# Optimization experiments

Measured on AMD Instinct MI355X. Metric: run time of the kernel, lower is better.

The kernel has to match this reference:

```python
import jax, jax.numpy as jnp
import numpy as np

F32 = jnp.float32

def denorm_px(pts, H, W):
    # kornia denormalize_pixel_coordinates: [-1,1] -> pixel
    x = (pts[..., 0] + 1.0) * (W - 1) * 0.5
    y = (pts[..., 1] + 1.0) * (H - 1) * 0.5
    return jnp.stack([x, y], axis=-1)

def norm_px(pts, H, W):
    x = pts[..., 0] * 2.0 / (W - 1) - 1.0
    y = pts[..., 1] * 2.0 / (H - 1) - 1.0
    return jnp.stack([x, y], axis=-1)

def conv2d_same(x, k, mode):
    # depthwise 2d conv, 'same' output, border via jnp.pad mode
    kh, kw = k.shape
    ph, pw = kh // 2, kw // 2
    xp = jnp.pad(x, ((0, 0), (0, 0), (ph, ph), (pw, pw)), mode=mode)
    C = x.shape[1]
    kern = jnp.broadcast_to(k[None, None], (C, 1, kh, kw)).astype(x.dtype)
    return jax.lax.conv_general_dilated(xp, kern, (1, 1), 'VALID',
        dimension_numbers=('NCHW', 'OIHW', 'NCHW'), feature_group_count=C)

def nms2d(x, k=5):
    p = k // 2
    m = jax.lax.reduce_window(x, -jnp.inf, jax.lax.max, (1, 1, k, k), (1, 1, 1, 1),
                              [(0, 0), (0, 0), (p, p), (p, p)])
    return jnp.where(x == m, x, 0.0)

def gaussian_kernel2d(ksize=7, sigma=1.0):
    ax = jnp.arange(ksize, dtype=F32) - (ksize - 1) / 2.0
    g = jnp.exp(-0.5 * (ax / sigma) ** 2)
    g = g / g.sum()
    return jnp.outer(g, g)

def gftt_response(gray):
    # kornia CornerGFTT: normalized sobel grads, blurred structure tensor, min-eig
    sx = jnp.array([[-1, 0, 1], [-2, 0, 2], [-1, 0, 1]], F32) / 8.0
    gx = conv2d_same(gray, sx, 'edge')
    gy = conv2d_same(gray, sx.T, 'edge')
    g = gaussian_kernel2d(7, 1.0)
    dx2 = conv2d_same(gx * gx, g, 'reflect')
    dy2 = conv2d_same(gy * gy, g, 'reflect')
    dxy = conv2d_same(gx * gy, g, 'reflect')
    tr = dx2 + dy2
    disc = jnp.sqrt(jnp.clip((dx2 - dy2) ** 2 + 4.0 * dxy ** 2, 0.0))
    return 0.5 * (tr - disc)

def laplacian5(x):
    k = jnp.ones((5, 5), F32).at[2, 2].set(1.0 - 25.0)
    k = k / jnp.abs(k).sum()  # kornia normalized laplacian kernel
    return conv2d_same(x, k, 'reflect')

def pairwise_project(pts, depths, poses, K):
    # pts [B,N,2] normalized; poses [B,4,4] cam-to-world
    # returns proj [B(dst),B(src),N,2] normalized + vis [B,B,N]
    B, N, _ = pts.shape
    H, W = depths.shape[-2:]
    px = denorm_px(pts, H, W)
    xi = jnp.clip(jnp.round(px[..., 0]), 0, W - 1).astype(jnp.int32)
    yi = jnp.clip(jnp.round(px[..., 1]), 0, H - 1).astype(jnp.int32)
    d = depths[jnp.arange(B)[:, None], 0, yi, xi]  # [B,N]
    Kinv = jnp.linalg.inv(K)
    hom = jnp.concatenate([px, jnp.ones_like(px[..., :1])], axis=-1)
    cam = (hom @ Kinv.T) * d[..., None]  # [B,N,3]
    R, t = poses[:, :3, :3], poses[:, :3, 3]
    world = jnp.einsum('bij,bnj->bni', R, cam) + t[:, None]
    diff = world[None] - t[:, None, None]  # [i,j,n,3]
    cam2 = jnp.einsum('iab,ijna->ijnb', R, diff)  # R_i^T (world - t_i)
    uvw = cam2 @ K.T
    z = uvw[..., 2]
    zs = jnp.where(jnp.abs(z) > 1e-6, z, 1e-6)
    u, v = uvw[..., 0] / zs, uvw[..., 1] / zs
    vis = (z > 0.1) & (u >= 0) & (u <= W - 1) & (v >= 0) & (v <= H - 1)
    return norm_px(jnp.stack([u, v], -1), H, W), vis

def pairwise_cosine_inter(x, y, eps=1e-8):
    xx = jnp.sum(x * x, -1)
    yy = jnp.sum(y * y, -1)
    xy = jnp.einsum('amd,bnd->abmn', x, y)
    den = jnp.sqrt(jnp.clip(xx[:, None, :, None] * yy[None, :, None, :], eps * eps))
    return xy / den

def pairwise_cosine_intra(x, y, eps=1e-8):
    xx = jnp.sum(x * x, -1)
    yy = jnp.sum(y * y, -1)
    xy = jnp.einsum('bmd,bnd->bmn', x, y)
    den = jnp.sqrt(jnp.clip(xx[..., :, None] * yy[..., None, :], eps * eps))
    return xy / den

def distinction_loss(desc):
    return jnp.maximum(pairwise_cosine_intra(desc, desc), 0.0).mean()

def match_loss(desc, points, proj, vis, H, W, radius=1.0):
    B, N, _ = points.shape
    src = denorm_px(jax.lax.stop_gradient(points), H, W)  # [b,m,2]
    dst = denorm_px(jax.lax.stop_gradient(proj), H, W)  # [a,b,n,2]
    x2 = jnp.sum(src * src, -1)  # [b,m]
    y2 = jnp.sum(dst * dst, -1)  # [a,b,n]
    xy = jnp.einsum('bmd,abnd->abmn', src, dst)
    dist = jnp.sqrt(jnp.clip(x2[None, :, :, None] + y2[:, :, None, :] - 2.0 * xy, 0.0))
    valid = vis[:, :, :, None]  # torch: dist[invis rows] = nan -> excluded from both masks
    tri = jnp.triu(jnp.ones((N, N), bool), 1)
    pcos = pairwise_cosine_inter(desc, desc)
    mpos = (dist <= radius) & tri & valid
    mneg = (dist > radius) & tri & valid
    pos_mean = jnp.sum(jnp.where(mpos, pcos, 0.0)) / jnp.maximum(mpos.sum(), 1)
    neg_mean = jnp.sum(jnp.where(mneg, pcos, 0.0)) / jnp.maximum(mneg.sum(), 1)
    return 1.0 - pos_mean + neg_mean

def get_corner_target(imgs, depths, poses, K, num_corners=500, radius=8):
    B, _, H, W = imgs.shape
    gray = 0.299 * imgs[:, 0:1] + 0.587 * imgs[:, 1:2] + 0.114 * imgs[:, 2:3]
    corners = nms2d(gftt_response(gray), 5)
    # MaxPool(8, return_indices) + MaxUnpool(8): keep only per-8x8-block max
    xr = corners.reshape(B, 1, H // radius, radius, W // radius, radius)
    bm = xr.max(axis=(3, 5), keepdims=True)
    keep = jnp.where(xr == bm, xr, 0.0).reshape(B, 1, H, W)
    values, idx = jax.lax.top_k(keep.reshape(B, -1), num_corners)  # [B,Nc]
    coords = jnp.stack([idx % W, idx // W], axis=2).astype(F32)  # (x,y)
    coords = norm_px(coords, H, W)
    proj, vis = pairwise_project(coords, depths, poses, K)  # [B,B,Nc,2]
    proj = jnp.where(vis[..., None], proj, -2.0)
    comb = jnp.transpose(proj, (1, 0, 2, 3)).reshape(B, B * num_corners, 2)
    px = jnp.round(denorm_px(comb, H, W)).astype(jnp.int32)
    wf = px[..., 0].reshape(-1)
    hf = px[..., 1].reshape(-1)
    bf = jnp.repeat(jnp.arange(B), B * num_corners)
    vals = jnp.tile(values.reshape(-1), B)
    mask = (wf >= 0) & (hf >= 0) & (wf < W) & (hf < H)
    vals = jnp.where(mask, vals, 0.0)
    wf = jnp.clip(wf, 0, W - 1)
    hf = jnp.clip(hf, 0, H - 1)
    target = jnp.zeros_like(corners).at[bf, 0, hf, wf].max(vals)
    target = nms2d(target, 5)
    return jax.lax.stop_gradient((target > 0).astype(F32))

def score_loss(scores, imgs, depths, poses, K):
    target = get_corner_target(imgs, depths, poses, K)
    p = jnp.clip(scores, 1e-12, 1.0 - 1e-12)
    bce = -(target * jnp.log(p) + (1.0 - target) * jnp.log(1.0 - p)).mean()
    lap = laplacian5(scores)
    return bce + (scores * jnp.exp(-lap)).mean() * 10.0

def featurenet_loss(descriptors, points, pointness, depths_dense, poses, K, imgs):
    beta = (1.0, 0.5, 1.0)
    H, W = pointness.shape[2], pointness.shape[3]
    distinction = distinction_loss(descriptors)
    cornerness = score_loss(pointness, imgs, depths_dense, poses, K)
    proj_pts, vis = pairwise_project(points, depths_dense, poses, K)
    match = match_loss(descriptors, points, proj_pts, vis, H, W, radius=1.0)
    return beta[0] * distinction + beta[1] * cornerness + beta[2] * match

def setup_inputs() -> dict:
    key = jax.random.key(0)
    ks = jax.random.split(key, 6)
    B, N, D, H, W = 6, 1024, 128, 320, 320
    descriptors = jax.random.normal(ks[0], (B, N, D), F32)
    points = jax.random.uniform(ks[1], (B, N, 2), F32, -0.9, 0.9)
    pointness = jax.random.uniform(ks[2], (B, 1, H, W), F32, 1e-3, 1.0 - 1e-3)
    depths_dense = jax.random.uniform(ks[3], (B, 1, H, W), F32, 1.0, 6.0)
    t = jax.random.uniform(ks[4], (B, 3), F32, -0.2, 0.2)
    poses = jnp.tile(jnp.eye(4, dtype=F32), (B, 1, 1)).at[:, :3, 3].set(t)
    K = jnp.array([[float(W), 0.0, W / 2.0], [0.0, float(W), H / 2.0], [0.0, 0.0, 1.0]], F32)
    imgs = jax.random.uniform(ks[5], (B, 3, H, W), F32)
    return dict(descriptors=descriptors, points=points, pointness=pointness,
                depths_dense=depths_dense, poses=poses, K=K, imgs=imgs)

def reference(descriptors, points, pointness, depths_dense, poses, K, imgs):
    return featurenet_loss(descriptors, points, pointness, depths_dense, poses, K, imgs)
```

## Files before the change

### kernel.cpp

```cpp
#include <hip/hip_runtime.h>
#include <stdint.h>

#define BB 6
#define NPTS 1024
#define DD 128
#define HH 320
#define WW 320
#define NC 500
#define HWsz (HH*WW)
#define CAP 2048
#define NBLK ((HH/8)*(WW/8))
#define TX 32
#define TY 8
#define NSLOT 64

typedef __attribute__((ext_vector_type(8))) short bf16x8;
typedef __attribute__((ext_vector_type(4))) float f32x4;

__device__ __forceinline__ int clampi(int v, int lo, int hi){ return v<lo?lo:(v>hi?hi:v); }
__device__ __forceinline__ int refl(int p, int L){ if(p<0)p=-p; if(p>=L)p=2*L-2-p; return p; }

__device__ __forceinline__ float wave_sum(float v){
  #pragma unroll
  for (int o = 32; o > 0; o >>= 1) v += __shfl_xor(v, o, 64);
  return v;
}
__device__ __forceinline__ double wave_sumd(double v){
  #pragma unroll
  for (int o = 32; o > 0; o >>= 1) v += __shfl_xor(v, o, 64);
  return v;
}
__device__ __forceinline__ float wave_max(float v){
  #pragma unroll
  for (int o = 32; o > 0; o >>= 1) v = fmaxf(v, __shfl_xor(v, o, 64));
  return v;
}

__device__ __constant__ float GW[7] = {
  0.0044330481f, 0.0540055850f, 0.2420362300f, 0.3990502700f,
  0.2420362300f, 0.0540055850f, 0.0044330481f };

struct Proj { float u, v; int vis; };

__device__ Proj project_point(float ptx, float pty, int jsrc, int itgt,
                              const float* __restrict__ depths,
                              const float* __restrict__ poses,
                              const float* __restrict__ Km)
{
  float pxx = ((ptx + 1.0f)*(float)(WW-1))*0.5f;
  float pxy = ((pty + 1.0f)*(float)(HH-1))*0.5f;
  float rx = rintf(pxx), ry = rintf(pxy);
  rx = fminf(fmaxf(rx, 0.f), (float)(WW-1));
  ry = fminf(fmaxf(ry, 0.f), (float)(HH-1));
  int xi = (int)rx, yi = (int)ry;
  float d = depths[(size_t)jsrc*HWsz + yi*WW + xi];
  float a00=Km[0],a01=Km[1],a02=Km[2],a10=Km[3],a11=Km[4],a12=Km[5],a20=Km[6],a21=Km[7],a22=Km[8];
  float det = a00*(a11*a22 - a12*a21) - a01*(a10*a22 - a12*a20) + a02*(a10*a21 - a11*a20);
  float id_ = 1.0f/det;
  float i00 = (a11*a22 - a12*a21)*id_;
  float i01 = (a02*a21 - a01*a22)*id_;
  float i02 = (a01*a12 - a02*a11)*id_;
  float i10 = (a12*a20 - a10*a22)*id_;
  float i11 = (a00*a22 - a02*a20)*id_;
  float i12 = (a02*a10 - a00*a12)*id_;
  float i20 = (a10*a21 - a11*a20)*id_;
  float i21 = (a01*a20 - a00*a21)*id_;
  float i22 = (a00*a11 - a01*a10)*id_;
  float c0 = (i00*pxx + i01*pxy + i02)*d;
  float c1 = (i10*pxx + i11*pxy + i12)*d;
  float c2 = (i20*pxx + i21*pxy + i22)*d;
  const float* Pj = poses + (size_t)jsrc*16;
  float w0 = Pj[0]*c0 + Pj[1]*c1 + Pj[2]*c2  + Pj[3];
  float w1 = Pj[4]*c0 + Pj[5]*c1 + Pj[6]*c2  + Pj[7];
  float w2 = Pj[8]*c0 + Pj[9]*c1 + Pj[10]*c2 + Pj[11];
  const float* Pi = poses + (size_t)itgt*16;
  float dx = w0 - Pi[3], dy = w1 - Pi[7], dz = w2 - Pi[11];
  float e0 = Pi[0]*dx + Pi[4]*dy + Pi[8]*dz;
  float e1 = Pi[1]*dx + Pi[5]*dy + Pi[9]*dz;
  float e2 = Pi[2]*dx + Pi[6]*dy + Pi[10]*dz;
  float uu = a00*e0 + a01*e1 + a02*e2;
  float vv = a10*e0 + a11*e1 + a12*e2;
  float zz = a20*e0 + a21*e1 + a22*e2;
  float zs = (fabsf(zz) > 1e-6f) ? zz : 1e-6f;
  Proj r;
  r.u = uu/zs; r.v = vv/zs;
  r.vis = (zz > 0.1f) && (r.u >= 0.f) && (r.u <= (float)(WW-1)) && (r.v >= 0.f) && (r.v <= (float)(HH-1));
  return r;
}

__global__ void k_gray(const float* __restrict__ imgs, float* __restrict__ gray){
  int t = blockIdx.x*blockDim.x + threadIdx.x;
  if (t >= BB*HWsz) return;
  int b = t / HWsz, p = t - b*HWsz;
  const float* base = imgs + (size_t)b*3*HWsz;
  gray[t] = 0.299f*base[p] + 0.587f*base[HWsz+p] + 0.114f*base[2*HWsz+p];
}

__global__ void k_sobel(const float* __restrict__ gray, float* __restrict__ gxx,
                        float* __restrict__ gyy, float* __restrict__ gxy){
  int t = blockIdx.x*blockDim.x + threadIdx.x;
  if (t >= BB*HWsz) return;
  int b = t / HWsz, p = t - b*HWsz;
  int y = p / WW, x = p - y*WW;
  const float* g = gray + (size_t)b*HWsz;
  int ym = clampi(y-1,0,HH-1), yp = clampi(y+1,0,HH-1);
  int xm = clampi(x-1,0,WW-1), xp = clampi(x+1,0,WW-1);
  float g00 = g[ym*WW+xm], g01 = g[ym*WW+x], g02 = g[ym*WW+xp];
  float g10 = g[y*WW+xm],                    g12 = g[y*WW+xp];
  float g20 = g[yp*WW+xm], g21 = g[yp*WW+x], g22 = g[yp*WW+xp];
  float gx = 0.125f*(g02-g00) + 0.25f*(g12-g10) + 0.125f*(g22-g20);
  float gy = 0.125f*(g20-g00) + 0.25f*(g21-g01) + 0.125f*(g22-g02);
  gxx[t] = gx*gx; gyy[t] = gy*gy; gxy[t] = gx*gy;
}

__global__ __launch_bounds__(256) void k_gauss_resp(const float* __restrict__ gxx,
        const float* __restrict__ gyy, const float* __restrict__ gxy, float* __restrict__ resp){
  __shared__ float lxx[TY+6][TX+6], lyy[TY+6][TX+6], lxy[TY+6][TX+6];
  int b = blockIdx.z;
  int x0 = blockIdx.x*TX, y0 = blockIdx.y*TY;
  const float* axx = gxx + (size_t)b*HWsz;
  const float* ayy = gyy + (size_t)b*HWsz;
  const float* axy = gxy + (size_t)b*HWsz;
  const int W2 = TX+6, H2 = TY+6;
  for (int i = threadIdx.x; i < H2*W2; i += 256){
    int ly = i / W2, lx = i - ly*W2;
    int gy = refl(y0 - 3 + ly, HH), gx = refl(x0 - 3 + lx, WW);
    size_t off = (size_t)gy*WW + gx;
    lxx[ly][lx] = axx[off]; lyy[ly][lx] = ayy[off]; lxy[ly][lx] = axy[off];
  }
  __syncthreads();
  int tx = threadIdx.x & (TX-1), ty = threadIdx.x / TX;
  float sxx=0.f, syy=0.f, sxy=0.f;
  #pragma unroll
  for (int i=0;i<7;++i){
    float wr = GW[i];
    #pragma unroll
    for (int j=0;j<7;++j){
      float wc = wr*GW[j];
      sxx += wc*lxx[ty+i][tx+j];
      syy += wc*lyy[ty+i][tx+j];
      sxy += wc*lxy[ty+i][tx+j];
    }
  }
  float tr = sxx+syy, df = sxx-syy;
  float disc = sqrtf(fmaxf(df*df + 4.f*sxy*sxy, 0.f));
  resp[(size_t)b*HWsz + (size_t)(y0+ty)*WW + (x0+tx)] = 0.5f*(tr - disc);
}

__global__ __launch_bounds__(256) void k_nms5(const float* __restrict__ resp, float* __restrict__ keep){
  __shared__ float lr[TY+4][TX+4];
  int b = blockIdx.z;
  int x0 = blockIdx.x*TX, y0 = blockIdx.y*TY;
  const float* rb = resp + (size_t)b*HWsz;
  const int W2 = TX+4, H2 = TY+4;
  for (int i = threadIdx.x; i < H2*W2; i += 256){
    int ly = i / W2, lx = i - ly*W2;
    int gy = y0 - 2 + ly, gx = x0 - 2 + lx;
    lr[ly][lx] = (gy >= 0 && gy < HH && gx >= 0 && gx < WW) ? rb[(size_t)gy*WW + gx] : -1e30f;
  }
  __syncthreads();
  int tx = threadIdx.x & (TX-1), ty = threadIdx.x / TX;
  float m = -1e30f;
  #pragma unroll
  for (int dy=0; dy<5; ++dy)
    #pragma unroll
    for (int dx=0; dx<5; ++dx) m = fmaxf(m, lr[ty+dy][tx+dx]);
  float r = lr[ty+2][tx+2];
  keep[(size_t)b*HWsz + (size_t)(y0+ty)*WW + (x0+tx)] = (r == m) ? r : 0.f;
}

__global__ void k_blockmax_compact(const float* __restrict__ keep,
        unsigned long long* __restrict__ ckeys, unsigned int* __restrict__ ccnt){
  int gw = (blockIdx.x*(int)blockDim.x + (int)threadIdx.x) >> 6;
  int lane = threadIdx.x & 63;
  if (gw >= BB*NBLK) return;
  int b = gw / NBLK; int r = gw - b*NBLK;
  int by = r / (WW/8), bx = r - by*(WW/8);
  int yy = by*8 + (lane >> 3), xx2 = bx*8 + (lane & 7);
  float v = keep[(size_t)b*HWsz + (size_t)yy*WW + xx2];
  float bm = wave_max(v);
  if (!(bm > 0.f)) return;
  unsigned long long mask = __ballot(v == bm);
  if (v == bm){
    unsigned long long key =
      ((unsigned long long)__float_as_uint(bm) << 32) |
      (unsigned long long)(0xFFFFFFFFu - (unsigned int)(yy*WW + xx2));
    int rank = __popcll(mask & ((1ull << lane) - 1ull));
    if (rank == 0){
      ckeys[(size_t)b*CAP + r] = key;
    } else {
      unsigned int slot = NBLK + atomicAdd(&ccnt[b], 1u);
      if (slot < CAP) ckeys[(size_t)b*CAP + slot] = key;
    }
  }
}

__global__ __launch_bounds__(1024) void k_top500(const unsigned long long* __restrict__ ckeys,
        float* __restrict__ cpts, float* __restrict__ cvals){
  __shared__ unsigned long long sk[CAP];
  int b = blockIdx.x;
  int tid = threadIdx.x;
  for (int i = tid; i < CAP; i += 1024)
    sk[i] = ckeys[(size_t)b*CAP + i];
  __syncthreads();
  for (int k = 2; k <= CAP; k <<= 1){
    for (int j = k >> 1; j > 0; j >>= 1){
      for (int i = tid; i < CAP; i += 1024){
        int l = i ^ j;
        if (l > i){
          unsigned long long A = sk[i], Bv = sk[l];
          bool up = ((i & k) == 0);
          if ((A > Bv) == up){ sk[i] = Bv; sk[l] = A; }
        }
      }
      __syncthreads();
    }
  }
  if (tid < NC){
    unsigned long long key = sk[CAP-1-tid];
    float val = __uint_as_float((unsigned int)(key >> 32));
    size_t o = (size_t)b*NC + tid;
    if (val > 0.f){
      unsigned int idx = 0xFFFFFFFFu - (unsigned int)(key & 0xFFFFFFFFull);
      float fx = (float)(idx % WW), fy = (float)(idx / WW);
      cpts[o*2+0] = (fx*2.0f)/(float)(WW-1) - 1.0f;
      cpts[o*2+1] = (fy*2.0f)/(float)(HH-1) - 1.0f;
      cvals[o] = val;
    } else {
      cpts[o*2+0] = __int_as_float(0x7fc00000);
      cpts[o*2+1] = __int_as_float(0x7fc00000);
      cvals[o] = 0.f;
    }
  }
}

__global__ void k_corner_scatter(const float* __restrict__ cpts, const float* __restrict__ cvals,
        const float* __restrict__ depths, const float* __restrict__ poses,
        const float* __restrict__ Km, unsigned int* __restrict__ target){
  int t = blockIdx.x*blockDim.x + threadIdx.x;
  if (t >= BB*BB*NC) return;
  int i = t / (BB*NC); int r = t - i*(BB*NC); int j = r / NC; int n = r - j*NC;
  float val = cvals[(size_t)i*NC + n];
  float ptx = cpts[((size_t)j*NC+n)*2+0];
  float pty = cpts[((size_t)j*NC+n)*2+1];
  if (!(val > 0.f) || ptx != ptx) return;
  Proj pr = project_point(ptx, pty, j, i, depths, poses, Km);
  if (!pr.vis) return;
  float nu = (pr.u*2.0f)/(float)(WW-1) - 1.0f;
  float nv = (pr.v*2.0f)/(float)(HH-1) - 1.0f;
  float px2 = ((nu+1.0f)*(float)(WW-1))*0.5f;
  float py2 = ((nv+1.0f)*(float)(HH-1))*0.5f;
  float rx = rintf(px2), ry = rintf(py2);
  if (!(rx >= 0.f && ry >= 0.f && rx <= (float)(WW-1) && ry <= (float)(HH-1))) return;
  int wf = (int)rx, hf = (int)ry;
  atomicMax(&target[(size_t)j*HWsz + hf*WW + wf], __float_as_uint(val));
}

__global__ __launch_bounds__(256) void k_score_reduce(const float* __restrict__ target,
        const float* __restrict__ scores, double* __restrict__ accs){
  __shared__ float ltg[TY+4][TX+4], lsc[TY+4][TX+4];
  __shared__ float rbuf[4][2];
  int b = blockIdx.z;
  int x0 = blockIdx.x*TX, y0 = blockIdx.y*TY;
  const float* tg = target + (size_t)b*HWsz;
  const float* sb = scores + (size_t)b*HWsz;
  const int W2 = TX+4, H2 = TY+4;
  for (int i = threadIdx.x; i < H2*W2; i += 256){
    int ly = i / W2, lx = i - ly*W2;
    int gy = y0 - 2 + ly, gx = x0 - 2 + lx;
    ltg[ly][lx] = (gy >= 0 && gy < HH && gx >= 0 && gx < WW) ? tg[(size_t)gy*WW + gx] : -1e30f;
    lsc[ly][lx] = sb[(size_t)refl(gy,HH)*WW + refl(gx,WW)];
  }
  __syncthreads();
  int tx = threadIdx.x & (TX-1), ty = threadIdx.x / TX;
  float m = -1e30f, S5 = 0.f;
  #pragma unroll
  for (int dy=0; dy<5; ++dy)
    #pragma unroll
    for (int dx=0; dx<5; ++dx){
      m = fmaxf(m, ltg[ty+dy][tx+dx]);
      S5 += lsc[ty+dy][tx+dx];
    }
  float tv = ltg[ty+2][tx+2];
  float sc = lsc[ty+2][tx+2];
  float tb = (tv > 0.f && tv == m) ? 1.f : 0.f;
  float pc = fminf(fmaxf(sc, 1e-12f), 1.0f - 1e-12f);
  float bce = -(tb*logf(pc) + (1.f-tb)*logf(1.f-pc));
  float lap = (S5 - sc)*(1.0f/48.0f) - 0.5f*sc;
  float extra = sc*expf(-lap);
  bce = wave_sum(bce); extra = wave_sum(extra);
  int wave = threadIdx.x >> 6, lane = threadIdx.x & 63;
  if (lane == 0){ rbuf[wave][0] = bce; rbuf[wave][1] = extra; }
  __syncthreads();
  if (threadIdx.x == 0){
    int slot = (blockIdx.x + blockIdx.y*(WW/TX) + blockIdx.z*400) & (NSLOT-1);
    atomicAdd(&accs[(1*NSLOT + slot)*8], (double)(rbuf[0][0]+rbuf[1][0]+rbuf[2][0]+rbuf[3][0]));
    atomicAdd(&accs[(2*NSLOT + slot)*8], (double)(rbuf[0][1]+rbuf[1][1]+rbuf[2][1]+rbuf[3][1]));
  }
}

__global__ void k_rownorm_bf16(const float* __restrict__ desc, float* __restrict__ xx,
                               unsigned short* __restrict__ dbf){
  int t = blockIdx.x*blockDim.x + threadIdx.x;
  if (t >= BB*NPTS) return;
  const float* dptr = desc + (size_t)t*DD;
  unsigned short* optr = dbf + (size_t)t*DD;
  float s = 0.f;
  for (int d = 0; d < DD; d += 4){
    float4 v = *(const float4*)(dptr + d);
    s += v.x*v.x + v.y*v.y + v.z*v.z + v.w*v.w;
    unsigned int u0 = __float_as_uint(v.x); optr[d+0] = (unsigned short)((u0 + 0x7fffu + ((u0>>16)&1u)) >> 16);
    unsigned int u1 = __float_as_uint(v.y); optr[d+1] = (unsigned short)((u1 + 0x7fffu + ((u1>>16)&1u)) >> 16);
    unsigned int u2 = __float_as_uint(v.z); optr[d+2] = (unsigned short)((u2 + 0x7fffu + ((u2>>16)&1u)) >> 16);
    unsigned int u3 = __float_as_uint(v.w); optr[d+3] = (unsigned short)((u3 + 0x7fffu + ((u3>>16)&1u)) >> 16);
  }
  xx[t] = s;
}

__global__ void k_proj_points(const float* __restrict__ points, const float* __restrict__ depths,
        const float* __restrict__ poses, const float* __restrict__ Km,
        float* __restrict__ mproj, unsigned char* __restrict__ mvis){
  int t = blockIdx.x*blockDim.x + threadIdx.x;
  if (t >= BB*BB*NPTS) return;
  int i = t / (BB*NPTS); int r = t - i*(BB*NPTS); int j = r / NPTS; int n = r - j*NPTS;
  float ptx = points[((size_t)j*NPTS+n)*2+0];
  float pty = points[((size_t)j*NPTS+n)*2+1];
  Proj pr = project_point(ptx, pty, j, i, depths, poses, Km);
  mproj[(size_t)t*2+0] = (pr.u*2.0f)/(float)(WW-1) - 1.0f;
  mproj[(size_t)t*2+1] = (pr.v*2.0f)/(float)(HH-1) - 1.0f;
  mvis[t] = pr.vis ? 1 : 0;
}

__global__ __launch_bounds__(256) void k_distinction_mfma(const unsigned short* __restrict__ dbf,
        const float* __restrict__ xx, double* __restrict__ accs){
  __shared__ float rbuf[4];
  int b = blockIdx.z;
  int mt = blockIdx.x, nh = blockIdx.y;
  int tid = threadIdx.x;
  int wave = tid >> 6, lane = tid & 63;
  int wr = mt*64 + (wave&1)*32;
  int wco = (wave>>1)*32;
  int r = lane & 15, kg = lane >> 4;
  const unsigned short* descb = dbf + (size_t)b*NPTS*DD;
  const float* xb = xx + (size_t)b*NPTS;
  bf16x8 af[4][2];
  #pragma unroll
  for (int ks = 0; ks < 4; ++ks){
    int ko = ks*32 + kg*8;
    af[ks][0] = *(const bf16x8*)(descb + (size_t)(wr+r)*DD + ko);
    af[ks][1] = *(const bf16x8*)(descb + (size_t)(wr+16+r)*DD + ko);
  }
  float mxx[2][4];
  #pragma unroll
  for (int mi = 0; mi < 2; ++mi)
    #pragma unroll
    for (int j = 0; j < 4; ++j)
      mxx[mi][j] = xb[wr + mi*16 + 4*kg + j];
  float local = 0.f;
  for (int nt = nh*8; nt < nh*8+8; ++nt){
    int wc = nt*64 + wco;
    float xn0 = xb[wc + r], xn1 = xb[wc + 16 + r];
    f32x4 c00 = {}, c01 = {}, c10 = {}, c11 = {};
    #pragma unroll
    for (int ks = 0; ks < 4; ++ks){
      int ko = ks*32 + kg*8;
      bf16x8 b0 = *(const bf16x8*)(descb + (size_t)(wc+r)*DD + ko);
      bf16x8 b1 = *(const bf16x8*)(descb + (size_t)(wc+16+r)*DD + ko);
      c00 = __builtin_amdgcn_mfma_f32_16x16x32_bf16(af[ks][0], b0, c00, 0, 0, 0);
      c01 = __builtin_amdgcn_mfma_f32_16x16x32_bf16(af[ks][0], b1, c01, 0, 0, 0);
      c10 = __builtin_amdgcn_mfma_f32_16x16x32_bf16(af[ks][1], b0, c10, 0, 0, 0);
      c11 = __builtin_amdgcn_mfma_f32_16x16x32_bf16(af[ks][1], b1, c11, 0, 0, 0);
    }
    #pragma unroll
    for (int mi = 0; mi < 2; ++mi){
      #pragma unroll
      for (int j = 0; j < 4; ++j){
        float xm = mxx[mi][j];
        float v0 = (mi ? c10[j] : c00[j]);
        float v1 = (mi ? c11[j] : c01[j]);
        local += fmaxf(v0 / sqrtf(fmaxf(xm*xn0, 1e-16f)), 0.f);
        local += fmaxf(v1 / sqrtf(fmaxf(xm*xn1, 1e-16f)), 0.f);
      }
    }
  }
  local = wave_sum(local);
  if (lane == 0) rbuf[wave] = local;
  __syncthreads();
  if (tid == 0){
    int slot = (blockIdx.x + blockIdx.y*16 + blockIdx.z*32) & (NSLOT-1);
    atomicAdd(&accs[(0*NSLOT + slot)*8], (double)(rbuf[0]+rbuf[1]+rbuf[2]+rbuf[3]));
  }
}

__global__ __launch_bounds__(256) void k_match_mfma(const unsigned short* __restrict__ dbf,
        const float* __restrict__ xx, const float* __restrict__ points,
        const float* __restrict__ mproj, const unsigned char* __restrict__ mvis,
        double* __restrict__ accs){
  __shared__ float rbuf[4][4];
  int ab = blockIdx.z; int a = ab / BB, b = ab - a*BB;
  int pairIdx = blockIdx.x;
  int tid = threadIdx.x;
  int wave = tid >> 6, lane = tid & 63;
  int wro = (wave&1)*32, wco = (wave>>1)*32;
  int r = lane & 15, kg = lane >> 4;
  const unsigned short* descA = dbf + (size_t)a*NPTS*DD;
  const unsigned short* descB = dbf + (size_t)b*NPTS*DD;
  const float* xxa = xx + (size_t)a*NPTS;
  const float* xxb = xx + (size_t)b*NPTS;
  const float* pts = points + (size_t)b*NPTS*2;
  const float* mp  = mproj + (((size_t)a*BB+b)*NPTS)*2;
  const unsigned char* mv = mvis + ((size_t)a*BB+b)*NPTS;
  float pos = 0.f, neg = 0.f, pcf = 0.f, ncf = 0.f;
  #pragma unroll
  for (int seg = 0; seg < 2; ++seg){
    int mt = seg ? (15 - pairIdx) : pairIdx;
    int wr = mt*64 + wro;
    bf16x8 af[4][2];
    #pragma unroll
    for (int ks = 0; ks < 4; ++ks){
      int ko = ks*32 + kg*8;
      af[ks][0] = *(const bf16x8*)(descA + (size_t)(wr+r)*DD + ko);
      af[ks][1] = *(const bf16x8*)(descA + (size_t)(wr+16+r)*DD + ko);
    }
    float msx[2][4], msy[2][4], mx2[2][4], mxx[2][4];
    bool  mok[2][4];
    #pragma unroll
    for (int mi = 0; mi < 2; ++mi){
      #pragma unroll
      for (int j = 0; j < 4; ++j){
        int m = wr + mi*16 + 4*kg + j;
        mok[mi][j] = (mv[m] != 0);
        float px = pts[m*2+0], py = pts[m*2+1];
        float sx = ((px+1.f)*(float)(WW-1))*0.5f;
        float sy = ((py+1.f)*(float)(HH-1))*0.5f;
        msx[mi][j] = sx; msy[mi][j] = sy;
        mx2[mi][j] = sx*sx + sy*sy;
        mxx[mi][j] = xxa[m];
      }
    }
    for (int nt = mt; nt < 16; ++nt){
      int wc = nt*64 + wco;
      float nxxv[2], ndx[2], ndy[2], ny2[2];
      #pragma unroll
      for (int ni = 0; ni < 2; ++ni){
        int n = wc + ni*16 + r;
        nxxv[ni] = xxb[n];
        float qx = mp[n*2+0], qy = mp[n*2+1];
        float dx = ((qx+1.f)*(float)(WW-1))*0.5f;
        float dy = ((qy+1.f)*(float)(HH-1))*0.5f;
        ndx[ni] = dx; ndy[ni] = dy;
        ny2[ni] = dx*dx + dy*dy;
      }
      f32x4 c00 = {}, c01 = {}, c10 = {}, c11 = {};
      #pragma unroll
      for (int ks = 0; ks < 4; ++ks){
        int ko = ks*32 + kg*8;
        bf16x8 b0 = *(const bf16x8*)(descB + (size_t)(wc+r)*DD + ko);
        bf16x8 b1 = *(const bf16x8*)(descB + (size_t)(wc+16+r)*DD + ko);
        c00 = __builtin_amdgcn_mfma_f32_16x16x32_bf16(af[ks][0], b0, c00, 0, 0, 0);
        c01 = __builtin_amdgcn_mfma_f32_16x16x32_bf16(af[ks][0], b1, c01, 0, 0, 0);
        c10 = __builtin_amdgcn_mfma_f32_16x16x32_bf16(af[ks][1], b0, c10, 0, 0, 0);
        c11 = __builtin_amdgcn_mfma_f32_16x16x32_bf16(af[ks][1], b1, c11, 0, 0, 0);
      }
      #pragma unroll
      for (int mi = 0; mi < 2; ++mi){
        #pragma unroll
        for (int j = 0; j < 4; ++j){
          if (!mok[mi][j]) continue;
          int m = wr + mi*16 + 4*kg + j;
          float sx = msx[mi][j], sy = msy[mi][j];
          float x2 = mx2[mi][j], xm = mxx[mi][j];
          #pragma unroll
          for (int ni = 0; ni < 2; ++ni){
            int n = wc + ni*16 + r;
            if (m >= n) continue;
            float dv = (mi ? (ni ? c11[j] : c10[j]) : (ni ? c01[j] : c00[j]));
            float d2 = x2 + ny2[ni] - 2.f*(sx*ndx[ni] + sy*ndy[ni]);
            float den = sqrtf(fmaxf(xm * nxxv[ni], 1e-16f));
            float p = dv/den;
            if (d2 <= 1.0f){ pos += p; pcf += 1.f; }
            else           { neg += p; ncf += 1.f; }
          }
        }
      }
    }
  }
  pos = wave_sum(pos); neg = wave_sum(neg);
  pcf = wave_sum(pcf); ncf = wave_sum(ncf);
  if (lane == 0){ rbuf[wave][0] = pos; rbuf[wave][1] = neg; rbuf[wave][2] = pcf; rbuf[wave][3] = ncf; }
  __syncthreads();
  if (tid == 0){
    int slot = (blockIdx.x + blockIdx.z*8) & (NSLOT-1);
    atomicAdd(&accs[(3*NSLOT + slot)*8], (double)(rbuf[0][0]+rbuf[1][0]+rbuf[2][0]+rbuf[3][0]));
    atomicAdd(&accs[(4*NSLOT + slot)*8], (double)(rbuf[0][1]+rbuf[1][1]+rbuf[2][1]+rbuf[3][1]));
    atomicAdd(&accs[(5*NSLOT + slot)*8], (double)(rbuf[0][2]+rbuf[1][2]+rbuf[2][2]+rbuf[3][2]));
    atomicAdd(&accs[(6*NSLOT + slot)*8], (double)(rbuf[0][3]+rbuf[1][3]+rbuf[2][3]+rbuf[3][3]));
  }
}

__global__ void k_final(const double* __restrict__ accs, float* __restrict__ out){
  int lane = threadIdx.x;
  double tot[7];
  #pragma unroll
  for (int q = 0; q < 7; ++q)
    tot[q] = wave_sumd(accs[((size_t)q*NSLOT + lane)*8]);
  if (lane == 0){
    double distinction = tot[0] / (double)((long long)BB*NPTS*NPTS);
    double bce = tot[1] / (double)((long long)BB*HWsz);
    double extra = tot[2] / (double)((long long)BB*HWsz);
    double cornerness = bce + 10.0*extra;
    double pcd = tot[5] < 0.5 ? 1.0 : tot[5];
    double ncd = tot[6] < 0.5 ? 1.0 : tot[6];
    double pos_mean = tot[3] / pcd;
    double neg_mean = tot[4] / ncd;
    double match = 1.0 - pos_mean + neg_mean;
    out[0] = (float)(distinction + 0.5*cornerness + match);
  }
}

extern "C" void kernel_launch(void* const* d_in, const int* in_sizes, int n_in,
                              void* d_out, int out_size, void* d_ws, size_t ws_size,
                              hipStream_t stream) {
  (void)in_sizes; (void)n_in; (void)out_size; (void)ws_size;
  const float* desc   = (const float*)d_in[0];
  const float* points = (const float*)d_in[1];
  const float* scores = (const float*)d_in[2];
  const float* depths = (const float*)d_in[3];
  const float* poses  = (const float*)d_in[4];
  const float* Km     = (const float*)d_in[5];
  const float* imgs   = (const float*)d_in[6];
  float* out = (float*)d_out;

  const size_t S = (size_t)BB*HWsz;
  float* gray = (float*)d_ws;
  float* bx   = gray + S;
  float* by   = bx + S;
  float* bxy  = by + S;
  float* resp = gray;
  float* keep = bx;
  unsigned long long* ckeys = (unsigned long long*)(bxy + S);
  unsigned int* ccnt = (unsigned int*)(ckeys + (size_t)BB*CAP);
  double* accs = (double*)(ccnt + 8);
  float* cpts  = (float*)(accs + 7*NSLOT*8);
  float* cvals = cpts + (size_t)BB*NC*2;
  float* xx    = cvals + (size_t)BB*NC;
  float* mproj = xx + (size_t)BB*NPTS;
  unsigned char* mvis = (unsigned char*)(mproj + (size_t)BB*BB*NPTS*2);
  unsigned short* dbf = (unsigned short*)(mvis + (size_t)BB*BB*NPTS);

  const int npx = BB*HWsz;
  dim3 blk(256);
  dim3 gpx((npx + 255)/256);
  dim3 gtile(WW/TX, HH/TY, BB);

  k_gray<<<gpx, blk, 0, stream>>>(imgs, gray);
  k_sobel<<<gpx, blk, 0, stream>>>(gray, bx, by, bxy);
  k_gauss_resp<<<gtile, blk, 0, stream>>>(bx, by, bxy, resp);

  hipMemsetAsync(by, 0, S*sizeof(float), stream);
  hipMemsetAsync(ckeys, 0,
      (size_t)BB*CAP*sizeof(unsigned long long) + 8*sizeof(unsigned int) +
      (size_t)7*NSLOT*8*sizeof(double), stream);

  k_nms5<<<gtile, blk, 0, stream>>>(resp, keep);
  {
    int n = BB*NBLK*64;
    k_blockmax_compact<<<dim3((n+255)/256), blk, 0, stream>>>(keep, ckeys, ccnt);
  }
  k_top500<<<dim3(BB), dim3(1024), 0, stream>>>(ckeys, cpts, cvals);
  {
    int n = BB*BB*NC;
    k_corner_scatter<<<dim3((n+255)/256), blk, 0, stream>>>(cpts, cvals, depths, poses, Km,
                                                            (unsigned int*)by);
  }
  k_score_reduce<<<gtile, blk, 0, stream>>>(by, scores, accs);
  {
    int n = BB*NPTS;
    k_rownorm_bf16<<<dim3((n+255)/256), blk, 0, stream>>>(desc, xx, dbf);
  }
  {
    int n = BB*BB*NPTS;
    k_proj_points<<<dim3((n+255)/256), blk, 0, stream>>>(points, depths, poses, Km, mproj, mvis);
  }
  k_distinction_mfma<<<dim3(16, 2, BB), blk, 0, stream>>>(dbf, xx, accs);
  k_match_mfma<<<dim3(8, 1, BB*BB), blk, 0, stream>>>(dbf, xx, points, mproj, mvis, accs);
  k_final<<<dim3(1), dim3(64), 0, stream>>>(accs, out);
}
```

Baseline: 238.5 us.

## Assign one 64x64 output tile per block in distinction and match GEMM kernels

Both MFMA kernels drop the per-block loop over column tiles, and each block now computes a single 64x64 tile. Distinction launches 16x16xB blocks instead of 16x2xB. Match launches 136 upper-triangular tiles per pair, indexed with a small while-loop decode, instead of 8 balanced row pairs. The aim is to expose far more blocks to fill the GPU's compute units. In exchange, A-fragments and per-row metadata are reloaded for every tile rather than reused, and block launches and atomics increase.

```diff
diff --git a/kernel.cpp b/kernel.cpp
--- a/kernel.cpp
+++ b/kernel.cpp
@@ -335,52 +335,37 @@
         const float* __restrict__ xx, double* __restrict__ accs){
   __shared__ float rbuf[4];
   int b = blockIdx.z;
-  int mt = blockIdx.x, nh = blockIdx.y;
   int tid = threadIdx.x;
   int wave = tid >> 6, lane = tid & 63;
-  int wr = mt*64 + (wave&1)*32;
-  int wco = (wave>>1)*32;
+  int wr = blockIdx.x*64 + (wave&1)*32;
+  int wc = blockIdx.y*64 + (wave>>1)*32;
   int r = lane & 15, kg = lane >> 4;
   const unsigned short* descb = dbf + (size_t)b*NPTS*DD;
   const float* xb = xx + (size_t)b*NPTS;
-  bf16x8 af[4][2];
+  f32x4 c00 = {}, c01 = {}, c10 = {}, c11 = {};
   #pragma unroll
   for (int ks = 0; ks < 4; ++ks){
     int ko = ks*32 + kg*8;
-    af[ks][0] = *(const bf16x8*)(descb + (size_t)(wr+r)*DD + ko);
-    af[ks][1] = *(const bf16x8*)(descb + (size_t)(wr+16+r)*DD + ko);
-  }
-  float mxx[2][4];
-  #pragma unroll
-  for (int mi = 0; mi < 2; ++mi)
+    bf16x8 a0 = *(const bf16x8*)(descb + (size_t)(wr+r)*DD + ko);
+    bf16x8 a1 = *(const bf16x8*)(descb + (size_t)(wr+16+r)*DD + ko);
+    bf16x8 b0 = *(const bf16x8*)(descb + (size_t)(wc+r)*DD + ko);
+    bf16x8 b1 = *(const bf16x8*)(descb + (size_t)(wc+16+r)*DD + ko);
+    c00 = __builtin_amdgcn_mfma_f32_16x16x32_bf16(a0, b0, c00, 0, 0, 0);
+    c01 = __builtin_amdgcn_mfma_f32_16x16x32_bf16(a0, b1, c01, 0, 0, 0);
+    c10 = __builtin_amdgcn_mfma_f32_16x16x32_bf16(a1, b0, c10, 0, 0, 0);
+    c11 = __builtin_amdgcn_mfma_f32_16x16x32_bf16(a1, b1, c11, 0, 0, 0);
+  }
+  float xn0 = xb[wc + r], xn1 = xb[wc + 16 + r];
+  float local = 0.f;
+  #pragma unroll
+  for (int mi = 0; mi < 2; ++mi){
     #pragma unroll
-    for (int j = 0; j < 4; ++j)
-      mxx[mi][j] = xb[wr + mi*16 + 4*kg + j];
-  float local = 0.f;
-  for (int nt = nh*8; nt < nh*8+8; ++nt){
-    int wc = nt*64 + wco;
-    float xn0 = xb[wc + r], xn1 = xb[wc + 16 + r];
-    f32x4 c00 = {}, c01 = {}, c10 = {}, c11 = {};
-    #pragma unroll
-    for (int ks = 0; ks < 4; ++ks){
-      int ko = ks*32 + kg*8;
-      bf16x8 b0 = *(const bf16x8*)(descb + (size_t)(wc+r)*DD + ko);
-      bf16x8 b1 = *(const bf16x8*)(descb + (size_t)(wc+16+r)*DD + ko);
-      c00 = __builtin_amdgcn_mfma_f32_16x16x32_bf16(af[ks][0], b0, c00, 0, 0, 0);
-      c01 = __builtin_amdgcn_mfma_f32_16x16x32_bf16(af[ks][0], b1, c01, 0, 0, 0);
-      c10 = __builtin_amdgcn_mfma_f32_16x16x32_bf16(af[ks][1], b0, c10, 0, 0, 0);
-      c11 = __builtin_amdgcn_mfma_f32_16x16x32_bf16(af[ks][1], b1, c11, 0, 0, 0);
-    }
-    #pragma unroll
-    for (int mi = 0; mi < 2; ++mi){
-      #pragma unroll
-      for (int j = 0; j < 4; ++j){
-        float xm = mxx[mi][j];
-        float v0 = (mi ? c10[j] : c00[j]);
-        float v1 = (mi ? c11[j] : c01[j]);
-        local += fmaxf(v0 / sqrtf(fmaxf(xm*xn0, 1e-16f)), 0.f);
-        local += fmaxf(v1 / sqrtf(fmaxf(xm*xn1, 1e-16f)), 0.f);
-      }
+    for (int j = 0; j < 4; ++j){
+      float xm = xb[wr + mi*16 + 4*kg + j];
+      float v0 = (mi ? c10[j] : c00[j]);
+      float v1 = (mi ? c11[j] : c01[j]);
+      local += fmaxf(v0 / sqrtf(fmaxf(xm*xn0, 1e-16f)), 0.f);
+      local += fmaxf(v1 / sqrtf(fmaxf(xm*xn1, 1e-16f)), 0.f);
     }
   }
   local = wave_sum(local);
@@ -398,10 +383,14 @@
         double* __restrict__ accs){
   __shared__ float rbuf[4][4];
   int ab = blockIdx.z; int a = ab / BB, b = ab - a*BB;
-  int pairIdx = blockIdx.x;
+  int ti = blockIdx.x;
+  int mt = 0;
+  while (ti >= 16 - mt){ ti -= 16 - mt; ++mt; }
+  int nt = mt + ti;
   int tid = threadIdx.x;
   int wave = tid >> 6, lane = tid & 63;
-  int wro = (wave&1)*32, wco = (wave>>1)*32;
+  int wr = mt*64 + (wave&1)*32;
+  int wc = nt*64 + (wave>>1)*32;
   int r = lane & 15, kg = lane >> 4;
   const unsigned short* descA = dbf + (size_t)a*NPTS*DD;
   const unsigned short* descB = dbf + (size_t)b*NPTS*DD;
@@ -410,78 +399,52 @@
   const float* pts = points + (size_t)b*NPTS*2;
   const float* mp  = mproj + (((size_t)a*BB+b)*NPTS)*2;
   const unsigned char* mv = mvis + ((size_t)a*BB+b)*NPTS;
+  f32x4 c00 = {}, c01 = {}, c10 = {}, c11 = {};
+  #pragma unroll
+  for (int ks = 0; ks < 4; ++ks){
+    int ko = ks*32 + kg*8;
+    bf16x8 a0 = *(const bf16x8*)(descA + (size_t)(wr+r)*DD + ko);
+    bf16x8 a1 = *(const bf16x8*)(descA + (size_t)(wr+16+r)*DD + ko);
+    bf16x8 b0 = *(const bf16x8*)(descB + (size_t)(wc+r)*DD + ko);
+    bf16x8 b1 = *(const bf16x8*)(descB + (size_t)(wc+16+r)*DD + ko);
+    c00 = __builtin_amdgcn_mfma_f32_16x16x32_bf16(a0, b0, c00, 0, 0, 0);
+    c01 = __builtin_amdgcn_mfma_f32_16x16x32_bf16(a0, b1, c01, 0, 0, 0);
+    c10 = __builtin_amdgcn_mfma_f32_16x16x32_bf16(a1, b0, c10, 0, 0, 0);
+    c11 = __builtin_amdgcn_mfma_f32_16x16x32_bf16(a1, b1, c11, 0, 0, 0);
+  }
+  float nxxv[2], ndx[2], ndy[2], ny2[2];
+  #pragma unroll
+  for (int ni = 0; ni < 2; ++ni){
+    int n = wc + ni*16 + r;
+    nxxv[ni] = xxb[n];
+    float qx = mp[n*2+0], qy = mp[n*2+1];
+    float dx = ((qx+1.f)*(float)(WW-1))*0.5f;
+    float dy = ((qy+1.f)*(float)(HH-1))*0.5f;
+    ndx[ni] = dx; ndy[ni] = dy;
+    ny2[ni] = dx*dx + dy*dy;
+  }
   float pos = 0.f, neg = 0.f, pcf = 0.f, ncf = 0.f;
   #pragma unroll
-  for (int seg = 0; seg < 2; ++seg){
-    int mt = seg ? (15 - pairIdx) : pairIdx;
-    int wr = mt*64 + wro;
-    bf16x8 af[4][2];
+  for (int mi = 0; mi < 2; ++mi){
     #pragma unroll
-    for (int ks = 0; ks < 4; ++ks){
-      int ko = ks*32 + kg*8;
-      af[ks][0] = *(const bf16x8*)(descA + (size_t)(wr+r)*DD + ko);
-      af[ks][1] = *(const bf16x8*)(descA + (size_t)(wr+16+r)*DD + ko);
-    }
-    float msx[2][4], msy[2][4], mx2[2][4], mxx[2][4];
-    bool  mok[2][4];
-    #pragma unroll
-    for (int mi = 0; mi < 2; ++mi){
-      #pragma unroll
-      for (int j = 0; j < 4; ++j){
-        int m = wr + mi*16 + 4*kg + j;
-        mok[mi][j] = (mv[m] != 0);
-        float px = pts[m*2+0], py = pts[m*2+1];
-        float sx = ((px+1.f)*(float)(WW-1))*0.5f;
-        float sy = ((py+1.f)*(float)(HH-1))*0.5f;
-        msx[mi][j] = sx; msy[mi][j] = sy;
-        mx2[mi][j] = sx*sx + sy*sy;
-        mxx[mi][j] = xxa[m];
-      }
-    }
-    for (int nt = mt; nt < 16; ++nt){
-      int wc = nt*64 + wco;
-      float nxxv[2], ndx[2], ndy[2], ny2[2];
+    for (int j = 0; j < 4; ++j){
+      int m = wr + mi*16 + 4*kg + j;
+      if (!mv[m]) continue;
+      float px = pts[m*2+0], py = pts[m*2+1];
+      float sx = ((px+1.f)*(float)(WW-1))*0.5f;
+      float sy = ((py+1.f)*(float)(HH-1))*0.5f;
+      float x2 = sx*sx + sy*sy;
+      float xm = xxa[m];
       #pragma unroll
       for (int ni = 0; ni < 2; ++ni){
         int n = wc + ni*16 + r;
-        nxxv[ni] = xxb[n];
-        float qx = mp[n*2+0], qy = mp[n*2+1];
-        float dx = ((qx+1.f)*(float)(WW-1))*0.5f;
-        float dy = ((qy+1.f)*(float)(HH-1))*0.5f;
-        ndx[ni] = dx; ndy[ni] = dy;
-        ny2[ni] = dx*dx + dy*dy;
-      }
-      f32x4 c00 = {}, c01 = {}, c10 = {}, c11 = {};
-      #pragma unroll
-      for (int ks = 0; ks < 4; ++ks){
-        int ko = ks*32 + kg*8;
-        bf16x8 b0 = *(const bf16x8*)(descB + (size_t)(wc+r)*DD + ko);
-        bf16x8 b1 = *(const bf16x8*)(descB + (size_t)(wc+16+r)*DD + ko);
-        c00 = __builtin_amdgcn_mfma_f32_16x16x32_bf16(af[ks][0], b0, c00, 0, 0, 0);
-        c01 = __builtin_amdgcn_mfma_f32_16x16x32_bf16(af[ks][0], b1, c01, 0, 0, 0);
-        c10 = __builtin_amdgcn_mfma_f32_16x16x32_bf16(af[ks][1], b0, c10, 0, 0, 0);
-        c11 = __builtin_amdgcn_mfma_f32_16x16x32_bf16(af[ks][1], b1, c11, 0, 0, 0);
-      }
-      #pragma unroll
-      for (int mi = 0; mi < 2; ++mi){
-        #pragma unroll
-        for (int j = 0; j < 4; ++j){
-          if (!mok[mi][j]) continue;
-          int m = wr + mi*16 + 4*kg + j;
-          float sx = msx[mi][j], sy = msy[mi][j];
-          float x2 = mx2[mi][j], xm = mxx[mi][j];
-          #pragma unroll
-          for (int ni = 0; ni < 2; ++ni){
-            int n = wc + ni*16 + r;
-            if (m >= n) continue;
-            float dv = (mi ? (ni ? c11[j] : c10[j]) : (ni ? c01[j] : c00[j]));
-            float d2 = x2 + ny2[ni] - 2.f*(sx*ndx[ni] + sy*ndy[ni]);
-            float den = sqrtf(fmaxf(xm * nxxv[ni], 1e-16f));
-            float p = dv/den;
-            if (d2 <= 1.0f){ pos += p; pcf += 1.f; }
-            else           { neg += p; ncf += 1.f; }
-          }
-        }
+        if (m >= n) continue;
+        float dv = (mi ? (ni ? c11[j] : c10[j]) : (ni ? c01[j] : c00[j]));
+        float d2 = x2 + ny2[ni] - 2.f*(sx*ndx[ni] + sy*ndy[ni]);
+        float den = sqrtf(fmaxf(xm * nxxv[ni], 1e-16f));
+        float p = dv/den;
+        if (d2 <= 1.0f){ pos += p; pcf += 1.f; }
+        else           { neg += p; ncf += 1.f; }
       }
     }
   }
@@ -582,7 +545,7 @@
     int n = BB*BB*NPTS;
     k_proj_points<<<dim3((n+255)/256), blk, 0, stream>>>(points, depths, poses, Km, mproj, mvis);
   }
-  k_distinction_mfma<<<dim3(16, 2, BB), blk, 0, stream>>>(dbf, xx, accs);
-  k_match_mfma<<<dim3(8, 1, BB*BB), blk, 0, stream>>>(dbf, xx, points, mproj, mvis, accs);
+  k_distinction_mfma<<<dim3(16, 16, BB), blk, 0, stream>>>(dbf, xx, accs);
+  k_match_mfma<<<dim3(136, 1, BB*BB), blk, 0, stream>>>(dbf, xx, points, mproj, mvis, accs);
   k_final<<<dim3(1), dim3(64), 0, stream>>>(accs, out);
 }
```

Result: faster. 231.7 us (-2.8%).
